# Performance work log

Measured on AMD Instinct MI355X. Metric: run time of the kernel, lower is better.

Reference implementation:

```python
import jax, jax.numpy as jnp
import numpy as np
from jax import lax

VOCAB, ENC_DIM, PRED_H, JOINT_H = 4096, 1024, 640, 640
T, MAX_SYM, BLANK, SOS = 128, 30, 0, -1
S = T * (MAX_SYM + 1)  # upper bound on greedy-decode loop iterations


def setup_inputs() -> dict:
    key = jax.random.key(0)
    ks = jax.random.split(key, 10)
    rn = lambda k, shape, s: jax.random.normal(k, shape, jnp.float32) * s
    return {
        "enc_out": rn(ks[0], (1, T, ENC_DIM), 1.0),
        "out_len": T,
        "emb": rn(ks[1], (VOCAB, PRED_H), 0.1),
        "Wih0": rn(ks[2], (4 * PRED_H, PRED_H), 0.04),
        "Whh0": rn(ks[3], (4 * PRED_H, PRED_H), 0.04),
        "b0": jnp.zeros((4 * PRED_H,), jnp.float32),
        "Wih1": rn(ks[4], (4 * PRED_H, PRED_H), 0.04),
        "Whh1": rn(ks[5], (4 * PRED_H, PRED_H), 0.04),
        "b1": jnp.zeros((4 * PRED_H,), jnp.float32),
        "Wj1": rn(ks[6], (JOINT_H, ENC_DIM + PRED_H), 0.03),
        "bj1": jnp.zeros((JOINT_H,), jnp.float32),
        "Wj2": rn(ks[7], (VOCAB, JOINT_H), 0.04),
        "bj2": jnp.zeros((VOCAB,), jnp.float32),
    }


def _lstm_cell(x, h, c, Wih, Whh, b):
    z = x @ Wih.T + h @ Whh.T + b  # [4H], torch gate order i,f,g,o
    i, f, g, o = jnp.split(z, 4)
    c2 = jax.nn.sigmoid(f) * c + jax.nn.sigmoid(i) * jnp.tanh(g)
    return jax.nn.sigmoid(o) * jnp.tanh(c2), c2


def _decode(enc_out, timesteps, emb, Wih0, Whh0, b0, Wih1, Whh1, b1, Wj1, bj1, Wj2, bj2):
    enc = enc_out[0]  # [T, ENC_DIM]

    def step(carry, _):
        t, sa, last, h0, c0, h1, c1, labels, cnt, done = carry
        # prediction net step (SOS = -1 -> zero embedding)
        g_in = jnp.where(last < 0, 0.0, emb[jnp.maximum(last, 0)])
        h0n, c0n = _lstm_cell(g_in, h0, c0, Wih0, Whh0, b0)
        h1n, c1n = _lstm_cell(h0n, h1, c1, Wih1, Whh1, b1)
        # joint net on current encoder frame
        f = enc[jnp.minimum(t, T - 1)]
        hid = jax.nn.relu(Wj1 @ jnp.concatenate([f, h1n]) + bj1)
        logits = Wj2 @ hid + bj2  # [VOCAB]
        k = jnp.argmax(logits).astype(jnp.int32)
        stop_sym = (k == BLANK) | (sa >= MAX_SYM)
        emit = (~stop_sym) & (~done)
        adv = stop_sym & (~done)
        # emit: append symbol, keep hidden'; blank/max: advance time, discard hidden'
        last2 = jnp.where(emit, k, last)
        h0 = jnp.where(emit, h0n, h0); c0 = jnp.where(emit, c0n, c0)
        h1 = jnp.where(emit, h1n, h1); c1 = jnp.where(emit, c1n, c1)
        labels = labels.at[cnt].set(jnp.where(emit, k, labels[cnt]))
        cnt2 = cnt + emit.astype(jnp.int32)
        sa2 = jnp.where(emit, sa + 1, jnp.where(adv, 0, sa))
        t2 = t + adv.astype(jnp.int32)
        done2 = done | (adv & (t2 >= timesteps))
        out_logits = jnp.where(done, 0.0, logits)
        return (t2, sa2, last2, h0, c0, h1, c1, labels, cnt2, done2), out_logits

    zeros = jnp.zeros((PRED_H,), jnp.float32)
    carry0 = (jnp.int32(0), jnp.int32(0), jnp.int32(SOS),
              zeros, zeros, zeros, zeros,
              jnp.full((S,), -1, jnp.int32), jnp.int32(0), jnp.bool_(False))
    carry, logits_seq = lax.scan(step, carry0, None, length=S)
    labels, cnt = carry[7], carry[8]
    return logits_seq, labels, cnt


def reference(enc_out, out_len, emb, Wih0, Whh0, b0, Wih1, Whh1, b1, Wj1, bj1, Wj2, bj2):
    return _decode(enc_out, out_len, emb, Wih0, Whh0, b0, Wih1, Whh1, b1, Wj1, bj1, Wj2, bj2)
```

## Files before the change

### kernel.cpp

```cpp
#include <hip/hip_runtime.h>
#include <cmath>

#define VOCAB   4096
#define ENC_DIM 1024
#define PRED_H  640
#define JOINT_H 640
#define TMAX    128
#define MAX_SYM 30
#define NSTEPS  (TMAX*(MAX_SYM+1))
#define NWG     256
#define NTHR    512
#define RLX __ATOMIC_RELAXED
#define AGT __HIP_MEMORY_SCOPE_AGENT

typedef unsigned long long u64;


__device__ __forceinline__ float wave_red(float v){
  v += __shfl_xor(v, 32, 64);
  v += __shfl_xor(v, 16, 64);
  v += __shfl_xor(v,  8, 64);
  v += __shfl_xor(v,  4, 64);
  v += __shfl_xor(v,  2, 64);
  v += __shfl_xor(v,  1, 64);
  return v;
}

__device__ __forceinline__ float sigf(float x){ return 1.0f/(1.0f+expf(-x)); }

__device__ __forceinline__ void tstore(u64* p, float v, unsigned tag){
  __hip_atomic_store(p, ((u64)tag<<32) | (u64)__float_as_uint(v), RLX, AGT);
}
__device__ __forceinline__ float tpollv(u64* p, unsigned tag){
  u64 e = __hip_atomic_load(p, RLX, AGT);
  while ((unsigned)(e>>32) != tag){
    __builtin_amdgcn_s_sleep(4);
    e = __hip_atomic_load(p, RLX, AGT);
  }
  return __uint_as_float((unsigned)e);
}

__device__ __forceinline__ u64 mkentry(float lg, int r, unsigned ep){
  unsigned u = __float_as_uint(lg);
  u = (u & 0x80000000u) ? ~u : (u | 0x80000000u);
  return ((u64)u<<24) | ((u64)(ep&0xFFFu)<<12) | (u64)(4095 - r);
}

__global__ void init_ws(unsigned* ws){
  for (int i = threadIdx.x; i < 8192; i += 256) ws[i] = 0u;
}

__global__ __launch_bounds__(NTHR, 2)
void rnnt_decode(const float* __restrict__ enc,
                 const int*   __restrict__ outlen_p,
                 const float* __restrict__ emb,
                 const float* __restrict__ Wih0, const float* __restrict__ Whh0, const float* __restrict__ b0,
                 const float* __restrict__ Wih1, const float* __restrict__ Whh1, const float* __restrict__ b1,
                 const float* __restrict__ Wj1,  const float* __restrict__ bj1,
                 const float* __restrict__ Wj2,  const float* __restrict__ bj2,
                 float* __restrict__ out,
                 u64* __restrict__ parts,
                 u64* __restrict__ bufsT,
                 u64* __restrict__ hidT)
{
  const int wg = blockIdx.x, tid = threadIdx.x;
  const int wave = tid >> 6, lane = tid & 63;
  const int timesteps = outlen_p[0];

  __shared__ float xa[PRED_H];
  __shared__ float xsh[ENC_DIM];
  __shared__ float h0buf[2][PRED_H];
  __shared__ float h1buf[2][PRED_H];
  __shared__ float hidsh[JOINT_H];
  __shared__ float zsh[4][4];
  __shared__ float zjs[8];
  __shared__ float c0c[4], c1c[4], c0p[4], c1p[4];
  __shared__ u64 psh[8];
  __shared__ u64 pmx[4];

  const int jb = (wg*PRED_H)/NWG;
  const int je = ((wg+1)*PRED_H)/NWG;
  const int nj = je - jb;

  const int riA = wave, riB = wave + 8;
  const int gA = riA & 3, jA = riA >> 2;
  const int gB = riB & 3, jBx = riB >> 2;
  const bool hasB = (riB < 4*nj);
  const int rowA = gA*PRED_H + jb + jA;
  const int rowB = hasB ? (gB*PRED_H + jb + jBx) : 0;

  float w0xA[10], w0hA[10], w0xB[10], w0hB[10];
  float w1xA[10], w1hA[10], w1xB[10], w1hB[10];
  #pragma unroll
  for (int i = 0; i < 10; ++i){
    int c = lane + (i<<6);
    w0xA[i] = Wih0[(size_t)rowA*PRED_H + c];
    w0hA[i] = Whh0[(size_t)rowA*PRED_H + c];
    w1xA[i] = Wih1[(size_t)rowA*PRED_H + c];
    w1hA[i] = Whh1[(size_t)rowA*PRED_H + c];
    w0xB[i] = hasB ? Wih0[(size_t)rowB*PRED_H + c] : 0.f;
    w0hB[i] = hasB ? Whh0[(size_t)rowB*PRED_H + c] : 0.f;
    w1xB[i] = hasB ? Wih1[(size_t)rowB*PRED_H + c] : 0.f;
    w1hB[i] = hasB ? Whh1[(size_t)rowB*PRED_H + c] : 0.f;
  }
  const float bA0 = b0[rowA], bA1 = b1[rowA];
  const float bB0 = hasB ? b0[rowB] : 0.f, bB1 = hasB ? b1[rowB] : 0.f;

  const int vt = (wave < 4) ? wave*64 + lane : (wave-4)*64 + lane;
  float wjf0[4], wjh0[3], wjf2[4], wjh2[3];
  {
    int r0 = (wave < 4) ? jb : jb + 1;
    #pragma unroll
    for (int i = 0; i < 4; ++i) wjf0[i] = Wj1[(size_t)r0*(ENC_DIM+PRED_H) + vt + (i<<8)];
    #pragma unroll
    for (int i = 0; i < 3; ++i){
      int c = vt + (i<<8);
      wjh0[i] = (c < PRED_H) ? Wj1[(size_t)r0*(ENC_DIM+PRED_H) + ENC_DIM + c] : 0.f;
    }
    #pragma unroll
    for (int i = 0; i < 4; ++i) wjf2[i] = 0.f;
    #pragma unroll
    for (int i = 0; i < 3; ++i) wjh2[i] = 0.f;
    if (wave < 4 && nj == 3){
      int r2 = jb + 2;
      #pragma unroll
      for (int i = 0; i < 4; ++i) wjf2[i] = Wj1[(size_t)r2*(ENC_DIM+PRED_H) + vt + (i<<8)];
      #pragma unroll
      for (int i = 0; i < 3; ++i){
        int c = vt + (i<<8);
        wjh2[i] = (c < PRED_H) ? Wj1[(size_t)r2*(ENC_DIM+PRED_H) + ENC_DIM + c] : 0.f;
      }
    }
  }
  float bjr[3];
  bjr[0] = bj1[jb]; bjr[1] = bj1[jb+1]; bjr[2] = (nj == 3) ? bj1[jb+2] : 0.f;
  float ca0 = 0.f, ca2 = 0.f;

  const int rA2 = wg*16 + wave*2, rB2 = rA2 + 1;
  float wj2A[10], wj2B[10];
  #pragma unroll
  for (int i = 0; i < 10; ++i){
    int c = lane + (i<<6);
    wj2A[i] = Wj2[(size_t)rA2*JOINT_H + c];
    wj2B[i] = Wj2[(size_t)rB2*JOINT_H + c];
  }
  const float bjA2 = bj2[rA2], bjB2 = bj2[rB2];

  for (int i = tid; i < PRED_H; i += NTHR){ h0buf[0][i] = 0.f; h1buf[0][i] = 0.f; }
  if (tid < 4){ c0c[tid] = 0.f; c1c[tid] = 0.f; }
  __syncthreads();

  int cur = 0, t = 0, sa = 0, last = -1, cnt = 0, tStaged = -1;
  bool done = false, reuse = false;

  for (int s = 0; s < NSTEPS; ++s){
    if (done){
      if (wg < 8) out[(size_t)s*VOCAB + wg*NTHR + tid] = 0.f;
      continue;
    }
    const unsigned tag = (unsigned)(s + 1);

    if (!reuse){
      for (int i = tid; i < PRED_H; i += NTHR)
        xa[i] = (last >= 0) ? emb[(size_t)last*PRED_H + i] : 0.f;
      __syncthreads();
      {
        float acc = 0.f;
        #pragma unroll
        for (int i = 0; i < 10; ++i) acc = fmaf(w0xA[i], xa[lane+(i<<6)], acc);
        #pragma unroll
        for (int i = 0; i < 10; ++i) acc = fmaf(w0hA[i], h0buf[cur][lane+(i<<6)], acc);
        acc = wave_red(acc);
        if (lane == 0) zsh[gA][jA] = acc + bA0;
        if (hasB){
          float a2 = 0.f;
          #pragma unroll
          for (int i = 0; i < 10; ++i) a2 = fmaf(w0xB[i], xa[lane+(i<<6)], a2);
          #pragma unroll
          for (int i = 0; i < 10; ++i) a2 = fmaf(w0hB[i], h0buf[cur][lane+(i<<6)], a2);
          a2 = wave_red(a2);
          if (lane == 0) zsh[gB][jBx] = a2 + bB0;
        }
      }
      __syncthreads();
      if (tid < nj){
        float ig = sigf(zsh[0][tid]), fg = sigf(zsh[1][tid]);
        float gg = tanhf(zsh[2][tid]), og = sigf(zsh[3][tid]);
        float c2 = fg*c0c[tid] + ig*gg;
        c0p[tid] = c2;
        tstore(&bufsT[jb+tid], og*tanhf(c2), tag);
      }
      __syncthreads();

      for (int i = tid; i < PRED_H; i += NTHR)
        h0buf[cur^1][i] = tpollv(&bufsT[i], tag);
      __syncthreads();
      {
        float acc = 0.f;
        #pragma unroll
        for (int i = 0; i < 10; ++i) acc = fmaf(w1xA[i], h0buf[cur^1][lane+(i<<6)], acc);
        #pragma unroll
        for (int i = 0; i < 10; ++i) acc = fmaf(w1hA[i], h1buf[cur][lane+(i<<6)], acc);
        acc = wave_red(acc);
        if (lane == 0) zsh[gA][jA] = acc + bA1;
        if (hasB){
          float a2 = 0.f;
          #pragma unroll
          for (int i = 0; i < 10; ++i) a2 = fmaf(w1xB[i], h0buf[cur^1][lane+(i<<6)], a2);
          #pragma unroll
          for (int i = 0; i < 10; ++i) a2 = fmaf(w1hB[i], h1buf[cur][lane+(i<<6)], a2);
          a2 = wave_red(a2);
          if (lane == 0) zsh[gB][jBx] = a2 + bB1;
        }
      }
      __syncthreads();
      if (tid < nj){
        float ig = sigf(zsh[0][tid]), fg = sigf(zsh[1][tid]);
        float gg = tanhf(zsh[2][tid]), og = sigf(zsh[3][tid]);
        float c2 = fg*c1c[tid] + ig*gg;
        c1p[tid] = c2;
        tstore(&bufsT[PRED_H+jb+tid], og*tanhf(c2), tag);
      }
    }

    {
      int tcap = (t < TMAX-1) ? t : (TMAX-1);
      bool fNew = (tcap != tStaged);
      if (fNew)
        for (int i = tid; i < ENC_DIM; i += NTHR) xsh[i] = enc[(size_t)tcap*ENC_DIM + i];
      if (!reuse)
        for (int i = tid; i < PRED_H; i += NTHR)
          h1buf[cur^1][i] = tpollv(&bufsT[PRED_H+i], tag);
      __syncthreads();
      if (fNew){
        float a = 0.f;
        #pragma unroll
        for (int i = 0; i < 4; ++i) a = fmaf(wjf0[i], xsh[vt+(i<<8)], a);
        ca0 = a;
        if (wave < 4 && nj == 3){
          float a2 = 0.f;
          #pragma unroll
          for (int i = 0; i < 4; ++i) a2 = fmaf(wjf2[i], xsh[vt+(i<<8)], a2);
          ca2 = a2;
        }
        tStaged = tcap;
      }
      {
        float acc = ca0;
        #pragma unroll
        for (int i = 0; i < 3; ++i){
          int c = vt + (i<<8);
          acc = fmaf(wjh0[i], h1buf[cur^1][(c < PRED_H) ? c : 0], acc);
        }
        acc = wave_red(acc);
        if (lane == 0) zjs[wave] = acc;
      }
      __syncthreads();
      if (tid == 0){
        float v0 = zjs[0]+zjs[1]+zjs[2]+zjs[3] + bjr[0];
        tstore(&hidT[jb],   v0 > 0.f ? v0 : 0.f, tag);
        float v1 = zjs[4]+zjs[5]+zjs[6]+zjs[7] + bjr[1];
        tstore(&hidT[jb+1], v1 > 0.f ? v1 : 0.f, tag);
      }
      if (nj == 3){
        __syncthreads();
        if (wave < 4){
          float acc = ca2;
          #pragma unroll
          for (int i = 0; i < 3; ++i){
            int c = vt + (i<<8);
            acc = fmaf(wjh2[i], h1buf[cur^1][(c < PRED_H) ? c : 0], acc);
          }
          acc = wave_red(acc);
          if (lane == 0) zjs[wave] = acc;
        }
        __syncthreads();
        if (tid == 0){
          float v2 = zjs[0]+zjs[1]+zjs[2]+zjs[3] + bjr[2];
          tstore(&hidT[jb+2], v2 > 0.f ? v2 : 0.f, tag);
        }
      }
    }

    int k;
    {
      for (int i = tid; i < JOINT_H; i += NTHR)
        hidsh[i] = tpollv(&hidT[i], tag);
      __syncthreads();
      float accA = 0.f, accB = 0.f;
      #pragma unroll
      for (int i = 0; i < 10; ++i){
        float h = hidsh[lane+(i<<6)];
        accA = fmaf(wj2A[i], h, accA);
        accB = fmaf(wj2B[i], h, accB);
      }
      accA = wave_red(accA);
      accB = wave_red(accB);
      if (lane == 0){
        float lgA = accA + bjA2, lgB = accB + bjB2;
        out[(size_t)s*VOCAB + rA2] = lgA;
        out[(size_t)s*VOCAB + rB2] = lgB;
        u64 eA = mkentry(lgA, rA2, tag), eB = mkentry(lgB, rB2, tag);
        psh[wave] = eA > eB ? eA : eB;
      }
      __syncthreads();
      if (tid == 0){
        u64 m = psh[0];
        #pragma unroll
        for (int w = 1; w < 8; ++w) if (psh[w] > m) m = psh[w];
        __hip_atomic_store(&parts[wg], m, RLX, AGT);
      }
      u64 myp = 0;
      if (tid < 256){
        u64 e = __hip_atomic_load(&parts[tid], RLX, AGT);
        while ((unsigned)((e>>12) & 0xFFFu) != (tag & 0xFFFu)){
          __builtin_amdgcn_s_sleep(2);
          e = __hip_atomic_load(&parts[tid], RLX, AGT);
        }
        myp = e;
      }
      if (wave < 4){
        #pragma unroll
        for (int off = 32; off; off >>= 1){
          u64 o = __shfl_xor(myp, off, 64);
          if (o > myp) myp = o;
        }
        if (lane == 0) pmx[wave] = myp;
      }
      __syncthreads();
      u64 m = pmx[0];
      if (pmx[1] > m) m = pmx[1];
      if (pmx[2] > m) m = pmx[2];
      if (pmx[3] > m) m = pmx[3];
      k = 4095 - (int)(m & 0xFFFull);
    }

    bool stop = (k == 0) || (sa >= MAX_SYM);
    if (!stop){
      if (wg == 0 && tid == 0) out[(size_t)NSTEPS*VOCAB + cnt] = (float)k;
      if (tid < nj){ c0c[tid] = c0p[tid]; c1c[tid] = c1p[tid]; }
      cnt++; sa++; last = k; cur ^= 1; reuse = false;
    } else {
      sa = 0; t++; reuse = true;
      if (t >= timesteps) done = true;
    }
    __syncthreads();
  }

  size_t lab = (size_t)NSTEPS*VOCAB;
  int gidx = wg*NTHR + tid;
  for (int i = cnt + gidx; i < NSTEPS; i += NWG*NTHR) out[lab + i] = -1.f;
  if (wg == 0 && tid == 0) out[lab + NSTEPS] = (float)cnt;
}

extern "C" void kernel_launch(void* const* d_in, const int* in_sizes, int n_in,
                              void* d_out, int out_size, void* d_ws, size_t ws_size,
                              hipStream_t stream) {
  const float* enc  = (const float*)d_in[0];
  const int*   olen = (const int*)  d_in[1];
  const float* emb  = (const float*)d_in[2];
  const float* Wih0 = (const float*)d_in[3];
  const float* Whh0 = (const float*)d_in[4];
  const float* b0   = (const float*)d_in[5];
  const float* Wih1 = (const float*)d_in[6];
  const float* Whh1 = (const float*)d_in[7];
  const float* b1   = (const float*)d_in[8];
  const float* Wj1  = (const float*)d_in[9];
  const float* bj1  = (const float*)d_in[10];
  const float* Wj2  = (const float*)d_in[11];
  const float* bj2  = (const float*)d_in[12];
  float* out = (float*)d_out;

  u64* parts = (u64*)d_ws;
  u64* bufsT = (u64*)((char*)d_ws + 4096);
  u64* hidT  = (u64*)((char*)d_ws + 16384);

  init_ws<<<1, 256, 0, stream>>>((unsigned*)d_ws);

  void* args[] = {&enc,&olen,&emb,&Wih0,&Whh0,&b0,&Wih1,&Whh1,&b1,
                  &Wj1,&bj1,&Wj2,&bj2,&out,&parts,&bufsT,&hidT};
  hipLaunchCooperativeKernel((const void*)rnnt_decode, dim3(NWG), dim3(NTHR),
                             args, 0, stream);
}
```

Measured before the change: 51.19 ms.

## Halve workgroup count, widen per-WG work, and vectorize cross-WG tag polling

The decode kernel is repartitioned from 256 to 128 cooperative workgroups. Each one now owns 5 LSTM hidden units, 5 joint-hidden rows and 32 vocabulary rows, with more weights held in registers per wave. Polling of the shared h0/h1/hid buffers now uses 128-bit cache-bypassing loads that check two tagged entries at once. The argmax gather is reduced to a single wave reading 128 partials. The aim is to cut per-step grid synchronisation and polling latency in this latency-bound loop, at the cost of more serial work and higher register pressure per workgroup.

```diff
diff --git a/kernel.cpp b/kernel.cpp
--- a/kernel.cpp
+++ b/kernel.cpp
@@ -8,12 +8,13 @@
 #define TMAX    128
 #define MAX_SYM 30
 #define NSTEPS  (TMAX*(MAX_SYM+1))
-#define NWG     256
+#define NWG     128
 #define NTHR    512
 #define RLX __ATOMIC_RELAXED
 #define AGT __HIP_MEMORY_SCOPE_AGENT
 
 typedef unsigned long long u64;
+typedef __attribute__((ext_vector_type(4))) unsigned int uint4v;
 
 
 __device__ __forceinline__ float wave_red(float v){
@@ -31,13 +32,40 @@
 __device__ __forceinline__ void tstore(u64* p, float v, unsigned tag){
   __hip_atomic_store(p, ((u64)tag<<32) | (u64)__float_as_uint(v), RLX, AGT);
 }
-__device__ __forceinline__ float tpollv(u64* p, unsigned tag){
-  u64 e = __hip_atomic_load(p, RLX, AGT);
-  while ((unsigned)(e>>32) != tag){
-    __builtin_amdgcn_s_sleep(4);
-    e = __hip_atomic_load(p, RLX, AGT);
-  }
-  return __uint_as_float((unsigned)e);
+
+__device__ __forceinline__ uint4v tload2(const u64* p){
+  uint4v r;
+  asm volatile("global_load_dwordx4 %0, %1, off sc0 sc1\n\t"
+               "s_waitcnt vmcnt(0)"
+               : "=v"(r) : "v"(p) : "memory");
+  return r;
+}
+
+__device__ __forceinline__ void poll_vec(u64* src, float* dst, int n_u64,
+                                         unsigned tag, int tid){
+  for (int i = tid; i < (n_u64 >> 1); i += NTHR){
+    u64* p = src + 2*i;
+    int spins = 0;
+    for(;;){
+      uint4v v = tload2(p);
+      if (v.y == tag && v.w == tag){
+        dst[2*i]   = __uint_as_float(v.x);
+        dst[2*i+1] = __uint_as_float(v.z);
+        break;
+      }
+      __builtin_amdgcn_s_sleep(2);
+      if (++spins > (1<<20)){
+        u64 a = __hip_atomic_load(p,   RLX, AGT);
+        u64 b = __hip_atomic_load(p+1, RLX, AGT);
+        if ((unsigned)(a>>32) == tag && (unsigned)(b>>32) == tag){
+          dst[2*i]   = __uint_as_float((unsigned)a);
+          dst[2*i+1] = __uint_as_float((unsigned)b);
+          break;
+        }
+        spins = 0;
+      }
+    }
+  }
 }
 
 __device__ __forceinline__ u64 mkentry(float lg, int r, unsigned ep){
@@ -72,82 +100,65 @@
   __shared__ float h0buf[2][PRED_H];
   __shared__ float h1buf[2][PRED_H];
   __shared__ float hidsh[JOINT_H];
-  __shared__ float zsh[4][4];
-  __shared__ float zjs[8];
-  __shared__ float c0c[4], c1c[4], c0p[4], c1p[4];
+  __shared__ float zsh[4][5];
+  __shared__ float zjs[8][3];
+  __shared__ float c0c[5], c1c[5], c0p[5], c1p[5];
+  __shared__ float bj1sh[5];
   __shared__ u64 psh[8];
-  __shared__ u64 pmx[4];
-
-  const int jb = (wg*PRED_H)/NWG;
-  const int je = ((wg+1)*PRED_H)/NWG;
-  const int nj = je - jb;
-
-  const int riA = wave, riB = wave + 8;
-  const int gA = riA & 3, jA = riA >> 2;
-  const int gB = riB & 3, jBx = riB >> 2;
-  const bool hasB = (riB < 4*nj);
-  const int rowA = gA*PRED_H + jb + jA;
-  const int rowB = hasB ? (gB*PRED_H + jb + jBx) : 0;
-
-  float w0xA[10], w0hA[10], w0xB[10], w0hB[10];
-  float w1xA[10], w1hA[10], w1xB[10], w1hB[10];
+  __shared__ int kshm;
+
+  const int jb = wg*5;
+
+  float w0x[3][10], w0h[3][10], w1x[3][10], w1h[3][10];
+  float bL0[3], bL1[3];
   #pragma unroll
-  for (int i = 0; i < 10; ++i){
-    int c = lane + (i<<6);
-    w0xA[i] = Wih0[(size_t)rowA*PRED_H + c];
-    w0hA[i] = Whh0[(size_t)rowA*PRED_H + c];
-    w1xA[i] = Wih1[(size_t)rowA*PRED_H + c];
-    w1hA[i] = Whh1[(size_t)rowA*PRED_H + c];
-    w0xB[i] = hasB ? Wih0[(size_t)rowB*PRED_H + c] : 0.f;
-    w0hB[i] = hasB ? Whh0[(size_t)rowB*PRED_H + c] : 0.f;
-    w1xB[i] = hasB ? Wih1[(size_t)rowB*PRED_H + c] : 0.f;
-    w1hB[i] = hasB ? Whh1[(size_t)rowB*PRED_H + c] : 0.f;
-  }
-  const float bA0 = b0[rowA], bA1 = b1[rowA];
-  const float bB0 = hasB ? b0[rowB] : 0.f, bB1 = hasB ? b1[rowB] : 0.f;
-
-  const int vt = (wave < 4) ? wave*64 + lane : (wave-4)*64 + lane;
-  float wjf0[4], wjh0[3], wjf2[4], wjh2[3];
-  {
-    int r0 = (wave < 4) ? jb : jb + 1;
+  for (int rr = 0; rr < 3; ++rr){
+    int ri = wave + (rr<<3);
+    bool act = (rr < 2) || (wave < 4);
+    int row = act ? ((ri&3)*PRED_H + jb + (ri>>2)) : 0;
     #pragma unroll
-    for (int i = 0; i < 4; ++i) wjf0[i] = Wj1[(size_t)r0*(ENC_DIM+PRED_H) + vt + (i<<8)];
+    for (int i = 0; i < 10; ++i){
+      int c = lane + (i<<6);
+      w0x[rr][i] = act ? Wih0[(size_t)row*PRED_H + c] : 0.f;
+      w0h[rr][i] = act ? Whh0[(size_t)row*PRED_H + c] : 0.f;
+      w1x[rr][i] = act ? Wih1[(size_t)row*PRED_H + c] : 0.f;
+      w1h[rr][i] = act ? Whh1[(size_t)row*PRED_H + c] : 0.f;
+    }
+    bL0[rr] = act ? b0[row] : 0.f;
+    bL1[rr] = act ? b1[row] : 0.f;
+  }
+
+  const int grp = wave >> 2;
+  const int vt  = ((wave & 3)<<6) | lane;
+  const int nrows = grp ? 2 : 3;
+  float wjf[3][4], wjh[3][3], ca[3];
+  #pragma unroll
+  for (int p = 0; p < 3; ++p){
+    ca[p] = 0.f;
+    bool act = p < nrows;
+    int r = act ? (jb + 2*p + grp) : 0;
+    #pragma unroll
+    for (int i = 0; i < 4; ++i)
+      wjf[p][i] = act ? Wj1[(size_t)r*(ENC_DIM+PRED_H) + vt + (i<<8)] : 0.f;
     #pragma unroll
     for (int i = 0; i < 3; ++i){
       int c = vt + (i<<8);
-      wjh0[i] = (c < PRED_H) ? Wj1[(size_t)r0*(ENC_DIM+PRED_H) + ENC_DIM + c] : 0.f;
-    }
+      wjh[p][i] = (act && c < PRED_H) ? Wj1[(size_t)r*(ENC_DIM+PRED_H) + ENC_DIM + c] : 0.f;
+    }
+  }
+
+  const int r2b = (wg<<5) + (wave<<2);
+  float wj2[4][10], bj2r[4];
+  #pragma unroll
+  for (int q = 0; q < 4; ++q){
     #pragma unroll
-    for (int i = 0; i < 4; ++i) wjf2[i] = 0.f;
-    #pragma unroll
-    for (int i = 0; i < 3; ++i) wjh2[i] = 0.f;
-    if (wave < 4 && nj == 3){
-      int r2 = jb + 2;
-      #pragma unroll
-      for (int i = 0; i < 4; ++i) wjf2[i] = Wj1[(size_t)r2*(ENC_DIM+PRED_H) + vt + (i<<8)];
-      #pragma unroll
-      for (int i = 0; i < 3; ++i){
-        int c = vt + (i<<8);
-        wjh2[i] = (c < PRED_H) ? Wj1[(size_t)r2*(ENC_DIM+PRED_H) + ENC_DIM + c] : 0.f;
-      }
-    }
-  }
-  float bjr[3];
-  bjr[0] = bj1[jb]; bjr[1] = bj1[jb+1]; bjr[2] = (nj == 3) ? bj1[jb+2] : 0.f;
-  float ca0 = 0.f, ca2 = 0.f;
-
-  const int rA2 = wg*16 + wave*2, rB2 = rA2 + 1;
-  float wj2A[10], wj2B[10];
-  #pragma unroll
-  for (int i = 0; i < 10; ++i){
-    int c = lane + (i<<6);
-    wj2A[i] = Wj2[(size_t)rA2*JOINT_H + c];
-    wj2B[i] = Wj2[(size_t)rB2*JOINT_H + c];
-  }
-  const float bjA2 = bj2[rA2], bjB2 = bj2[rB2];
+    for (int i = 0; i < 10; ++i)
+      wj2[q][i] = Wj2[(size_t)(r2b+q)*JOINT_H + lane + (i<<6)];
+    bj2r[q] = bj2[r2b+q];
+  }
 
   for (int i = tid; i < PRED_H; i += NTHR){ h0buf[0][i] = 0.f; h1buf[0][i] = 0.f; }
-  if (tid < 4){ c0c[tid] = 0.f; c1c[tid] = 0.f; }
+  if (tid < 5){ c0c[tid] = 0.f; c1c[tid] = 0.f; bj1sh[tid] = bj1[jb+tid]; }
   __syncthreads();
 
   int cur = 0, t = 0, sa = 0, last = -1, cnt = 0, tStaged = -1;
@@ -164,26 +175,22 @@
       for (int i = tid; i < PRED_H; i += NTHR)
         xa[i] = (last >= 0) ? emb[(size_t)last*PRED_H + i] : 0.f;
       __syncthreads();
-      {
-        float acc = 0.f;
-        #pragma unroll
-        for (int i = 0; i < 10; ++i) acc = fmaf(w0xA[i], xa[lane+(i<<6)], acc);
-        #pragma unroll
-        for (int i = 0; i < 10; ++i) acc = fmaf(w0hA[i], h0buf[cur][lane+(i<<6)], acc);
-        acc = wave_red(acc);
-        if (lane == 0) zsh[gA][jA] = acc + bA0;
-        if (hasB){
-          float a2 = 0.f;
-          #pragma unroll
-          for (int i = 0; i < 10; ++i) a2 = fmaf(w0xB[i], xa[lane+(i<<6)], a2);
-          #pragma unroll
-          for (int i = 0; i < 10; ++i) a2 = fmaf(w0hB[i], h0buf[cur][lane+(i<<6)], a2);
-          a2 = wave_red(a2);
-          if (lane == 0) zsh[gB][jBx] = a2 + bB0;
-        }
-      }
-      __syncthreads();
-      if (tid < nj){
+      #pragma unroll
+      for (int rr = 0; rr < 3; ++rr){
+        bool act = (rr < 2) || (wave < 4);
+        if (act){
+          int ri = wave + (rr<<3);
+          float acc = 0.f;
+          #pragma unroll
+          for (int i = 0; i < 10; ++i) acc = fmaf(w0x[rr][i], xa[lane+(i<<6)], acc);
+          #pragma unroll
+          for (int i = 0; i < 10; ++i) acc = fmaf(w0h[rr][i], h0buf[cur][lane+(i<<6)], acc);
+          acc = wave_red(acc);
+          if (lane == 0) zsh[ri&3][ri>>2] = acc + bL0[rr];
+        }
+      }
+      __syncthreads();
+      if (tid < 5){
         float ig = sigf(zsh[0][tid]), fg = sigf(zsh[1][tid]);
         float gg = tanhf(zsh[2][tid]), og = sigf(zsh[3][tid]);
         float c2 = fg*c0c[tid] + ig*gg;
@@ -192,29 +199,24 @@
       }
       __syncthreads();
 
-      for (int i = tid; i < PRED_H; i += NTHR)
-        h0buf[cur^1][i] = tpollv(&bufsT[i], tag);
-      __syncthreads();
-      {
-        float acc = 0.f;
-        #pragma unroll
-        for (int i = 0; i < 10; ++i) acc = fmaf(w1xA[i], h0buf[cur^1][lane+(i<<6)], acc);
-        #pragma unroll
-        for (int i = 0; i < 10; ++i) acc = fmaf(w1hA[i], h1buf[cur][lane+(i<<6)], acc);
-        acc = wave_red(acc);
-        if (lane == 0) zsh[gA][jA] = acc + bA1;
-        if (hasB){
-          float a2 = 0.f;
-          #pragma unroll
-          for (int i = 0; i < 10; ++i) a2 = fmaf(w1xB[i], h0buf[cur^1][lane+(i<<6)], a2);
-          #pragma unroll
-          for (int i = 0; i < 10; ++i) a2 = fmaf(w1hB[i], h1buf[cur][lane+(i<<6)], a2);
-          a2 = wave_red(a2);
-          if (lane == 0) zsh[gB][jBx] = a2 + bB1;
-        }
-      }
-      __syncthreads();
-      if (tid < nj){
+      poll_vec(bufsT, h0buf[cur^1], PRED_H, tag, tid);
+      __syncthreads();
+      #pragma unroll
+      for (int rr = 0; rr < 3; ++rr){
+        bool act = (rr < 2) || (wave < 4);
+        if (act){
+          int ri = wave + (rr<<3);
+          float acc = 0.f;
+          #pragma unroll
+          for (int i = 0; i < 10; ++i) acc = fmaf(w1x[rr][i], h0buf[cur^1][lane+(i<<6)], acc);
+          #pragma unroll
+          for (int i = 0; i < 10; ++i) acc = fmaf(w1h[rr][i], h1buf[cur][lane+(i<<6)], acc);
+          acc = wave_red(acc);
+          if (lane == 0) zsh[ri&3][ri>>2] = acc + bL1[rr];
+        }
+      }
+      __syncthreads();
+      if (tid < 5){
         float ig = sigf(zsh[0][tid]), fg = sigf(zsh[1][tid]);
         float gg = tanhf(zsh[2][tid]), og = sigf(zsh[3][tid]);
         float c2 = fg*c1c[tid] + ig*gg;
@@ -229,79 +231,64 @@
       if (fNew)
         for (int i = tid; i < ENC_DIM; i += NTHR) xsh[i] = enc[(size_t)tcap*ENC_DIM + i];
       if (!reuse)
-        for (int i = tid; i < PRED_H; i += NTHR)
-          h1buf[cur^1][i] = tpollv(&bufsT[PRED_H+i], tag);
+        poll_vec(bufsT + PRED_H, h1buf[cur^1], PRED_H, tag, tid);
       __syncthreads();
       if (fNew){
-        float a = 0.f;
         #pragma unroll
-        for (int i = 0; i < 4; ++i) a = fmaf(wjf0[i], xsh[vt+(i<<8)], a);
-        ca0 = a;
-        if (wave < 4 && nj == 3){
-          float a2 = 0.f;
-          #pragma unroll
-          for (int i = 0; i < 4; ++i) a2 = fmaf(wjf2[i], xsh[vt+(i<<8)], a2);
-          ca2 = a2;
+        for (int p = 0; p < 3; ++p){
+          if (p < nrows){
+            float a = 0.f;
+            #pragma unroll
+            for (int i = 0; i < 4; ++i) a = fmaf(wjf[p][i], xsh[vt+(i<<8)], a);
+            ca[p] = a;
+          }
         }
         tStaged = tcap;
       }
-      {
-        float acc = ca0;
-        #pragma unroll
-        for (int i = 0; i < 3; ++i){
-          int c = vt + (i<<8);
-          acc = fmaf(wjh0[i], h1buf[cur^1][(c < PRED_H) ? c : 0], acc);
-        }
-        acc = wave_red(acc);
-        if (lane == 0) zjs[wave] = acc;
-      }
-      __syncthreads();
-      if (tid == 0){
-        float v0 = zjs[0]+zjs[1]+zjs[2]+zjs[3] + bjr[0];
-        tstore(&hidT[jb],   v0 > 0.f ? v0 : 0.f, tag);
-        float v1 = zjs[4]+zjs[5]+zjs[6]+zjs[7] + bjr[1];
-        tstore(&hidT[jb+1], v1 > 0.f ? v1 : 0.f, tag);
-      }
-      if (nj == 3){
-        __syncthreads();
-        if (wave < 4){
-          float acc = ca2;
+      #pragma unroll
+      for (int p = 0; p < 3; ++p){
+        if (p < nrows){
+          float acc = ca[p];
           #pragma unroll
           for (int i = 0; i < 3; ++i){
             int c = vt + (i<<8);
-            acc = fmaf(wjh2[i], h1buf[cur^1][(c < PRED_H) ? c : 0], acc);
+            acc = fmaf(wjh[p][i], h1buf[cur^1][(c < PRED_H) ? c : 0], acc);
           }
           acc = wave_red(acc);
-          if (lane == 0) zjs[wave] = acc;
-        }
-        __syncthreads();
-        if (tid == 0){
-          float v2 = zjs[0]+zjs[1]+zjs[2]+zjs[3] + bjr[2];
-          tstore(&hidT[jb+2], v2 > 0.f ? v2 : 0.f, tag);
-        }
+          if (lane == 0) zjs[wave][p] = acc;
+        }
+      }
+      __syncthreads();
+      if (tid < 5){
+        int p = tid >> 1, g = tid & 1;
+        float v = zjs[(g<<2)][p] + zjs[(g<<2)+1][p] + zjs[(g<<2)+2][p] + zjs[(g<<2)+3][p]
+                + bj1sh[tid];
+        tstore(&hidT[jb+tid], v > 0.f ? v : 0.f, tag);
       }
     }
 
     int k;
     {
-      for (int i = tid; i < JOINT_H; i += NTHR)
-        hidsh[i] = tpollv(&hidT[i], tag);
-      __syncthreads();
-      float accA = 0.f, accB = 0.f;
+      poll_vec(hidT, hidsh, JOINT_H, tag, tid);
+      __syncthreads();
+      float a0 = 0.f, a1 = 0.f, a2 = 0.f, a3 = 0.f;
       #pragma unroll
       for (int i = 0; i < 10; ++i){
         float h = hidsh[lane+(i<<6)];
-        accA = fmaf(wj2A[i], h, accA);
-        accB = fmaf(wj2B[i], h, accB);
-      }
-      accA = wave_red(accA);
-      accB = wave_red(accB);
+        a0 = fmaf(wj2[0][i], h, a0);
+        a1 = fmaf(wj2[1][i], h, a1);
+        a2 = fmaf(wj2[2][i], h, a2);
+        a3 = fmaf(wj2[3][i], h, a3);
+      }
+      a0 = wave_red(a0); a1 = wave_red(a1); a2 = wave_red(a2); a3 = wave_red(a3);
       if (lane == 0){
-        float lgA = accA + bjA2, lgB = accB + bjB2;
-        out[(size_t)s*VOCAB + rA2] = lgA;
-        out[(size_t)s*VOCAB + rB2] = lgB;
-        u64 eA = mkentry(lgA, rA2, tag), eB = mkentry(lgB, rB2, tag);
-        psh[wave] = eA > eB ? eA : eB;
+        float l0 = a0 + bj2r[0], l1 = a1 + bj2r[1], l2 = a2 + bj2r[2], l3 = a3 + bj2r[3];
+        *(float4*)(out + (size_t)s*VOCAB + r2b) = make_float4(l0, l1, l2, l3);
+        u64 m = mkentry(l0, r2b, tag);
+        u64 e = mkentry(l1, r2b+1, tag); if (e > m) m = e;
+        e = mkentry(l2, r2b+2, tag);     if (e > m) m = e;
+        e = mkentry(l3, r2b+3, tag);     if (e > m) m = e;
+        psh[wave] = m;
       }
       __syncthreads();
       if (tid == 0){
@@ -310,35 +297,43 @@
         for (int w = 1; w < 8; ++w) if (psh[w] > m) m = psh[w];
         __hip_atomic_store(&parts[wg], m, RLX, AGT);
       }
-      u64 myp = 0;
-      if (tid < 256){
-        u64 e = __hip_atomic_load(&parts[tid], RLX, AGT);
-        while ((unsigned)((e>>12) & 0xFFFu) != (tag & 0xFFFu)){
+      if (wave == 0){
+        u64* p = &parts[lane<<1];
+        u64 e0, e1;
+        int spins = 0;
+        for(;;){
+          uint4v v = tload2(p);
+          if ((((v.x>>12)&0xFFFu) == (tag&0xFFFu)) &&
+              (((v.z>>12)&0xFFFu) == (tag&0xFFFu))){
+            e0 = ((u64)v.y<<32) | v.x;
+            e1 = ((u64)v.w<<32) | v.z;
+            break;
+          }
           __builtin_amdgcn_s_sleep(2);
-          e = __hip_atomic_load(&parts[tid], RLX, AGT);
-        }
-        myp = e;
-      }
-      if (wave < 4){
+          if (++spins > (1<<20)){
+            u64 a = __hip_atomic_load(p,   RLX, AGT);
+            u64 b = __hip_atomic_load(p+1, RLX, AGT);
+            if ((((unsigned)(a>>12))&0xFFFu) == (tag&0xFFFu) &&
+                (((unsigned)(b>>12))&0xFFFu) == (tag&0xFFFu)){ e0 = a; e1 = b; break; }
+            spins = 0;
+          }
+        }
+        u64 m = e0 > e1 ? e0 : e1;
         #pragma unroll
         for (int off = 32; off; off >>= 1){
-          u64 o = __shfl_xor(myp, off, 64);
-          if (o > myp) myp = o;
-        }
-        if (lane == 0) pmx[wave] = myp;
-      }
-      __syncthreads();
-      u64 m = pmx[0];
-      if (pmx[1] > m) m = pmx[1];
-      if (pmx[2] > m) m = pmx[2];
-      if (pmx[3] > m) m = pmx[3];
-      k = 4095 - (int)(m & 0xFFFull);
+          u64 o = __shfl_xor(m, off, 64);
+          if (o > m) m = o;
+        }
+        if (lane == 0) kshm = 4095 - (int)(m & 0xFFFull);
+      }
+      __syncthreads();
+      k = kshm;
     }
 
     bool stop = (k == 0) || (sa >= MAX_SYM);
     if (!stop){
       if (wg == 0 && tid == 0) out[(size_t)NSTEPS*VOCAB + cnt] = (float)k;
-      if (tid < nj){ c0c[tid] = c0p[tid]; c1c[tid] = c1p[tid]; }
+      if (tid < 5){ c0c[tid] = c0p[tid]; c1c[tid] = c1p[tid]; }
       cnt++; sa++; last = k; cur ^= 1; reuse = false;
     } else {
       sa = 0; t++; reuse = true;
@@ -373,7 +368,7 @@
 
   u64* parts = (u64*)d_ws;
   u64* bufsT = (u64*)((char*)d_ws + 4096);
-  u64* hidT  = (u64*)((char*)d_ws + 16384);
+  u64* hidT  = (u64*)((char*)d_ws + 14336);
 
   init_ws<<<1, 256, 0, stream>>>((unsigned*)d_ws);
 
```

Result: slower. 61.68 ms (+20.5%).

## Replicate cross-workgroup exchange buffers 8x to spread polling contention

Applied to the files above, without the earlier changes.

Each producer now writes its tagged hidden-state, joint-hidden and argmax-partial values into 8 replicated copies of the exchange buffers. Each group of 32 workgroups polls only its own replica, so fewer pollers hit the same cache lines. Spin sleep intervals are also shortened. In exchange, every producer issues 8x more atomic stores per step, and the workspace grows and needs a wider init kernel.

```diff
diff --git a/kernel.cpp b/kernel.cpp
--- a/kernel.cpp
+++ b/kernel.cpp
@@ -10,6 +10,7 @@
 #define NSTEPS  (TMAX*(MAX_SYM+1))
 #define NWG     256
 #define NTHR    512
+#define NREP    8
 #define RLX __ATOMIC_RELAXED
 #define AGT __HIP_MEMORY_SCOPE_AGENT
 
@@ -28,13 +29,18 @@
 
 __device__ __forceinline__ float sigf(float x){ return 1.0f/(1.0f+expf(-x)); }
 
-__device__ __forceinline__ void tstore(u64* p, float v, unsigned tag){
-  __hip_atomic_store(p, ((u64)tag<<32) | (u64)__float_as_uint(v), RLX, AGT);
-}
+__device__ __forceinline__ void tstore8(u64* base, int stride, int idx,
+                                        float v, unsigned tag){
+  u64 w = ((u64)tag<<32) | (u64)__float_as_uint(v);
+  #pragma unroll
+  for (int r = 0; r < NREP; ++r)
+    __hip_atomic_store(base + r*stride + idx, w, RLX, AGT);
+}
+
 __device__ __forceinline__ float tpollv(u64* p, unsigned tag){
   u64 e = __hip_atomic_load(p, RLX, AGT);
   while ((unsigned)(e>>32) != tag){
-    __builtin_amdgcn_s_sleep(4);
+    __builtin_amdgcn_s_sleep(2);
     e = __hip_atomic_load(p, RLX, AGT);
   }
   return __uint_as_float((unsigned)e);
@@ -47,7 +53,8 @@
 }
 
 __global__ void init_ws(unsigned* ws){
-  for (int i = threadIdx.x; i < 8192; i += 256) ws[i] = 0u;
+  int i = blockIdx.x*blockDim.x + threadIdx.x;
+  for (; i < 34816; i += gridDim.x*blockDim.x) ws[i] = 0u;
 }
 
 __global__ __launch_bounds__(NTHR, 2)
@@ -66,6 +73,10 @@
   const int wg = blockIdx.x, tid = threadIdx.x;
   const int wave = tid >> 6, lane = tid & 63;
   const int timesteps = outlen_p[0];
+  const int rep = wg >> 5;
+  u64* myParts = parts + rep*256;
+  u64* myBufs  = bufsT + rep*1280;
+  u64* myHid   = hidT  + rep*640;
 
   __shared__ float xa[PRED_H];
   __shared__ float xsh[ENC_DIM];
@@ -188,12 +199,12 @@
         float gg = tanhf(zsh[2][tid]), og = sigf(zsh[3][tid]);
         float c2 = fg*c0c[tid] + ig*gg;
         c0p[tid] = c2;
-        tstore(&bufsT[jb+tid], og*tanhf(c2), tag);
+        tstore8(bufsT, 1280, jb+tid, og*tanhf(c2), tag);
       }
       __syncthreads();
 
       for (int i = tid; i < PRED_H; i += NTHR)
-        h0buf[cur^1][i] = tpollv(&bufsT[i], tag);
+        h0buf[cur^1][i] = tpollv(&myBufs[i], tag);
       __syncthreads();
       {
         float acc = 0.f;
@@ -219,7 +230,7 @@
         float gg = tanhf(zsh[2][tid]), og = sigf(zsh[3][tid]);
         float c2 = fg*c1c[tid] + ig*gg;
         c1p[tid] = c2;
-        tstore(&bufsT[PRED_H+jb+tid], og*tanhf(c2), tag);
+        tstore8(bufsT, 1280, PRED_H+jb+tid, og*tanhf(c2), tag);
       }
     }
 
@@ -230,7 +241,7 @@
         for (int i = tid; i < ENC_DIM; i += NTHR) xsh[i] = enc[(size_t)tcap*ENC_DIM + i];
       if (!reuse)
         for (int i = tid; i < PRED_H; i += NTHR)
-          h1buf[cur^1][i] = tpollv(&bufsT[PRED_H+i], tag);
+          h1buf[cur^1][i] = tpollv(&myBufs[PRED_H+i], tag);
       __syncthreads();
       if (fNew){
         float a = 0.f;
@@ -258,9 +269,9 @@
       __syncthreads();
       if (tid == 0){
         float v0 = zjs[0]+zjs[1]+zjs[2]+zjs[3] + bjr[0];
-        tstore(&hidT[jb],   v0 > 0.f ? v0 : 0.f, tag);
+        tstore8(hidT, 640, jb,   v0 > 0.f ? v0 : 0.f, tag);
         float v1 = zjs[4]+zjs[5]+zjs[6]+zjs[7] + bjr[1];
-        tstore(&hidT[jb+1], v1 > 0.f ? v1 : 0.f, tag);
+        tstore8(hidT, 640, jb+1, v1 > 0.f ? v1 : 0.f, tag);
       }
       if (nj == 3){
         __syncthreads();
@@ -277,7 +288,7 @@
         __syncthreads();
         if (tid == 0){
           float v2 = zjs[0]+zjs[1]+zjs[2]+zjs[3] + bjr[2];
-          tstore(&hidT[jb+2], v2 > 0.f ? v2 : 0.f, tag);
+          tstore8(hidT, 640, jb+2, v2 > 0.f ? v2 : 0.f, tag);
         }
       }
     }
@@ -285,7 +296,7 @@
     int k;
     {
       for (int i = tid; i < JOINT_H; i += NTHR)
-        hidsh[i] = tpollv(&hidT[i], tag);
+        hidsh[i] = tpollv(&myHid[i], tag);
       __syncthreads();
       float accA = 0.f, accB = 0.f;
       #pragma unroll
@@ -308,14 +319,16 @@
         u64 m = psh[0];
         #pragma unroll
         for (int w = 1; w < 8; ++w) if (psh[w] > m) m = psh[w];
-        __hip_atomic_store(&parts[wg], m, RLX, AGT);
+        #pragma unroll
+        for (int r = 0; r < NREP; ++r)
+          __hip_atomic_store(&parts[r*256 + wg], m, RLX, AGT);
       }
       u64 myp = 0;
       if (tid < 256){
-        u64 e = __hip_atomic_load(&parts[tid], RLX, AGT);
+        u64 e = __hip_atomic_load(&myParts[tid], RLX, AGT);
         while ((unsigned)((e>>12) & 0xFFFu) != (tag & 0xFFFu)){
-          __builtin_amdgcn_s_sleep(2);
-          e = __hip_atomic_load(&parts[tid], RLX, AGT);
+          __builtin_amdgcn_s_sleep(1);
+          e = __hip_atomic_load(&myParts[tid], RLX, AGT);
         }
         myp = e;
       }
@@ -372,10 +385,10 @@
   float* out = (float*)d_out;
 
   u64* parts = (u64*)d_ws;
-  u64* bufsT = (u64*)((char*)d_ws + 4096);
-  u64* hidT  = (u64*)((char*)d_ws + 16384);
-
-  init_ws<<<1, 256, 0, stream>>>((unsigned*)d_ws);
+  u64* bufsT = (u64*)((char*)d_ws + 16384);
+  u64* hidT  = (u64*)((char*)d_ws + 98304);
+
+  init_ws<<<64, 256, 0, stream>>>((unsigned*)d_ws);
 
   void* args[] = {&enc,&olen,&emb,&Wih0,&Whh0,&b0,&Wih1,&Whh1,&b1,
                   &Wj1,&bj1,&Wj2,&bj2,&out,&parts,&bufsT,&hidT};
```

After: 56.06 ms. 9.5% more time.

## Batch tagged polling per thread and merge third joint row into main pass

Applied to the files above, without the earlier changes.

Replaces the per-element spin loop on tagged inter-workgroup buffers with a poll5 helper, where 128 threads (two waves) each load five consecutive entries and retry together. The sleep interval while polling drops. The third joint hidden row for workgroups with nj==3 is now computed in the same phase as the first two, using a separate shared array, which removes two __syncthreads from the critical path. This cuts barrier count and polling latency in the sequential decode loop, at the cost of fewer threads polling and more global load traffic while spinning.

```diff
diff --git a/kernel.cpp b/kernel.cpp
--- a/kernel.cpp
+++ b/kernel.cpp
@@ -31,13 +31,28 @@
 __device__ __forceinline__ void tstore(u64* p, float v, unsigned tag){
   __hip_atomic_store(p, ((u64)tag<<32) | (u64)__float_as_uint(v), RLX, AGT);
 }
-__device__ __forceinline__ float tpollv(u64* p, unsigned tag){
-  u64 e = __hip_atomic_load(p, RLX, AGT);
-  while ((unsigned)(e>>32) != tag){
-    __builtin_amdgcn_s_sleep(4);
-    e = __hip_atomic_load(p, RLX, AGT);
-  }
-  return __uint_as_float((unsigned)e);
+
+__device__ __forceinline__ void poll5(u64* src, float* dst, unsigned tag, int pt){
+  u64* p = src + pt*5;
+  u64 a0,a1,a2,a3,a4;
+  for(;;){
+    a0 = __hip_atomic_load(p+0, RLX, AGT);
+    a1 = __hip_atomic_load(p+1, RLX, AGT);
+    a2 = __hip_atomic_load(p+2, RLX, AGT);
+    a3 = __hip_atomic_load(p+3, RLX, AGT);
+    a4 = __hip_atomic_load(p+4, RLX, AGT);
+    bool ok = ((unsigned)(a0>>32) == tag) & ((unsigned)(a1>>32) == tag)
+            & ((unsigned)(a2>>32) == tag) & ((unsigned)(a3>>32) == tag)
+            & ((unsigned)(a4>>32) == tag);
+    if (ok) break;
+    __builtin_amdgcn_s_sleep(1);
+  }
+  float* d = dst + pt*5;
+  d[0] = __uint_as_float((unsigned)a0);
+  d[1] = __uint_as_float((unsigned)a1);
+  d[2] = __uint_as_float((unsigned)a2);
+  d[3] = __uint_as_float((unsigned)a3);
+  d[4] = __uint_as_float((unsigned)a4);
 }
 
 __device__ __forceinline__ u64 mkentry(float lg, int r, unsigned ep){
@@ -74,6 +89,7 @@
   __shared__ float hidsh[JOINT_H];
   __shared__ float zsh[4][4];
   __shared__ float zjs[8];
+  __shared__ float zjs2[4];
   __shared__ float c0c[4], c1c[4], c0p[4], c1p[4];
   __shared__ u64 psh[8];
   __shared__ u64 pmx[4];
@@ -192,8 +208,7 @@
       }
       __syncthreads();
 
-      for (int i = tid; i < PRED_H; i += NTHR)
-        h0buf[cur^1][i] = tpollv(&bufsT[i], tag);
+      if (wave < 2) poll5(bufsT, h0buf[cur^1], tag, tid);
       __syncthreads();
       {
         float acc = 0.f;
@@ -228,9 +243,9 @@
       bool fNew = (tcap != tStaged);
       if (fNew)
         for (int i = tid; i < ENC_DIM; i += NTHR) xsh[i] = enc[(size_t)tcap*ENC_DIM + i];
-      if (!reuse)
-        for (int i = tid; i < PRED_H; i += NTHR)
-          h1buf[cur^1][i] = tpollv(&bufsT[PRED_H+i], tag);
+      if (!reuse){
+        if (wave < 2) poll5(bufsT + PRED_H, h1buf[cur^1], tag, tid);
+      }
       __syncthreads();
       if (fNew){
         float a = 0.f;
@@ -254,6 +269,16 @@
         }
         acc = wave_red(acc);
         if (lane == 0) zjs[wave] = acc;
+      }
+      if (wave < 4 && nj == 3){
+        float acc = ca2;
+        #pragma unroll
+        for (int i = 0; i < 3; ++i){
+          int c = vt + (i<<8);
+          acc = fmaf(wjh2[i], h1buf[cur^1][(c < PRED_H) ? c : 0], acc);
+        }
+        acc = wave_red(acc);
+        if (lane == 0) zjs2[wave] = acc;
       }
       __syncthreads();
       if (tid == 0){
@@ -261,22 +286,8 @@
         tstore(&hidT[jb],   v0 > 0.f ? v0 : 0.f, tag);
         float v1 = zjs[4]+zjs[5]+zjs[6]+zjs[7] + bjr[1];
         tstore(&hidT[jb+1], v1 > 0.f ? v1 : 0.f, tag);
-      }
-      if (nj == 3){
-        __syncthreads();
-        if (wave < 4){
-          float acc = ca2;
-          #pragma unroll
-          for (int i = 0; i < 3; ++i){
-            int c = vt + (i<<8);
-            acc = fmaf(wjh2[i], h1buf[cur^1][(c < PRED_H) ? c : 0], acc);
-          }
-          acc = wave_red(acc);
-          if (lane == 0) zjs[wave] = acc;
-        }
-        __syncthreads();
-        if (tid == 0){
-          float v2 = zjs[0]+zjs[1]+zjs[2]+zjs[3] + bjr[2];
+        if (nj == 3){
+          float v2 = zjs2[0]+zjs2[1]+zjs2[2]+zjs2[3] + bjr[2];
           tstore(&hidT[jb+2], v2 > 0.f ? v2 : 0.f, tag);
         }
       }
@@ -284,8 +295,7 @@
 
     int k;
     {
-      for (int i = tid; i < JOINT_H; i += NTHR)
-        hidsh[i] = tpollv(&hidT[i], tag);
+      if (wave < 2) poll5(hidT, hidsh, tag, tid);
       __syncthreads();
       float accA = 0.f, accB = 0.f;
       #pragma unroll
@@ -312,12 +322,11 @@
       }
       u64 myp = 0;
       if (tid < 256){
-        u64 e = __hip_atomic_load(&parts[tid], RLX, AGT);
-        while ((unsigned)((e>>12) & 0xFFFu) != (tag & 0xFFFu)){
-          __builtin_amdgcn_s_sleep(2);
-          e = __hip_atomic_load(&parts[tid], RLX, AGT);
-        }
-        myp = e;
+        for(;;){
+          u64 e = __hip_atomic_load(&parts[tid], RLX, AGT);
+          if ((unsigned)((e>>12) & 0xFFFu) == (tag & 0xFFFu)){ myp = e; break; }
+          __builtin_amdgcn_s_sleep(1);
+        }
       }
       if (wave < 4){
         #pragma unroll
@@ -373,7 +382,7 @@
 
   u64* parts = (u64*)d_ws;
   u64* bufsT = (u64*)((char*)d_ws + 4096);
-  u64* hidT  = (u64*)((char*)d_ws + 16384);
+  u64* hidT  = (u64*)((char*)d_ws + 14336);
 
   init_ws<<<1, 256, 0, stream>>>((unsigned*)d_ws);
 
```

After: 65.02 ms. +27.0%, slower.
